# Performance work log

Hardware: AMD Instinct MI355X
Metric: run time of the kernel (lower is better)

The kernel has to match this reference:

```python
import jax, jax.numpy as jnp
import numpy as np

B, T, C = 4, 2048, 1024
H = 16
HD = C // H  # 64


def setup_inputs() -> dict:
    key = jax.random.key(0)
    k1, k2, k3 = jax.random.split(key, 3)
    x = jax.random.normal(k1, (B, T, C), dtype=jnp.float32)
    W_qkv = jax.random.normal(k2, (3 * C, C), dtype=jnp.float32) * (C ** -0.5)
    W_proj = jax.random.normal(k3, (C, C), dtype=jnp.float32) * (C ** -0.5)
    b_proj = jnp.zeros((C,), dtype=jnp.float32)
    return {"x": x, "W_qkv": W_qkv, "W_proj": W_proj, "b_proj": b_proj}


def reference(x, W_qkv, W_proj, b_proj):
    # qkv = x @ W_qkv.T : [B,T,3C]
    qkv = jnp.einsum('btc,oc->bto', x, W_qkv)
    # Faithful to torch: view(B,T,H,3*HD) then chunk last dim -> per-head q/k/v
    qkv = qkv.reshape(B, T, H, 3 * HD)
    q, k, v = jnp.split(qkv, 3, axis=-1)      # each [B,T,H,HD]
    q = q.transpose(0, 2, 1, 3)               # [B,H,T,HD]
    k = k.transpose(0, 2, 1, 3)
    v = v.transpose(0, 2, 1, 3)
    scale = HD ** -0.5
    att = jnp.einsum('bhqd,bhkd->bhqk', q, k) * scale  # [B,H,T,T]
    causal = jnp.tril(jnp.ones((T, T), dtype=bool))
    att = jnp.where(causal, att, -jnp.inf)
    att = jax.nn.softmax(att, axis=-1)
    out = jnp.einsum('bhqk,bhkd->bhqd', att, v)        # [B,H,T,HD]
    out = out.transpose(0, 2, 1, 3).reshape(B, T, C)
    out = jnp.einsum('btc,oc->bto', out, W_proj) + b_proj
    return out
```

## Files before the change

kernel.cpp:

```cpp
#include <hip/hip_runtime.h>
#include <stdint.h>

#define B_ 4
#define T_ 2048
#define C_ 1024
#define H_ 16
#define HD_ 64

typedef __attribute__((ext_vector_type(8))) short short8;
typedef __attribute__((ext_vector_type(4))) float f32x4;

typedef uint32_t __attribute__((address_space(3))) lds_u32;
typedef const uint32_t __attribute__((address_space(1))) glb_u32;

__device__ inline void async16(const void* g, void* l) {
    __builtin_amdgcn_global_load_lds((glb_u32*)g, (lds_u32*)l, 16, 0, 0);
}

__device__ inline short f2bf(float f) {
    union { float f; uint32_t u; } x; x.f = f;
    uint32_t r = (x.u + 0x7fffu + ((x.u >> 16) & 1u)) >> 16;
    return (short)r;
}
__device__ inline float bf2f(short b) {
    union { uint32_t u; float f; } x; x.u = ((uint32_t)(uint16_t)b) << 16;
    return x.f;
}
__device__ inline uint32_t cvt_pk_bf16(float lo, float hi) {
    uint32_t r;
    asm("v_cvt_pk_bf16_f32 %0, %1, %2" : "=v"(r) : "v"(lo), "v"(hi));
    return r;
}

#define FENCE asm volatile("" ::: "memory")
#define BAR   do { FENCE; __builtin_amdgcn_s_barrier(); FENCE; } while (0)
#define VMC3  asm volatile("s_waitcnt vmcnt(3)" ::: "memory")

__global__ void convert_all(const void* __restrict__ x,  const void* __restrict__ wq,
                            const void* __restrict__ wp, const void* __restrict__ bias,
                            short* __restrict__ xd, short* __restrict__ wqd,
                            short* __restrict__ wpd, short* __restrict__ biasd,
                            int* __restrict__ flag_out)
{
    __shared__ int cnt;
    if (threadIdx.x == 0) cnt = 0;
    __syncthreads();
    int sane = 0;
    const uint32_t* xu = (const uint32_t*)x;
    for (int i = threadIdx.x; i < 1024; i += 256) {
        float v = bf2f((short)(xu[i] & 0xFFFFu));
        float a = fabsf(v);
        if (a > 1e-5f && a < 1e5f) sane++;
    }
    atomicAdd(&cnt, sane);
    __syncthreads();
    const int isf32 = (cnt < 512) ? 1 : 0;

    const int blk = blockIdx.x;
    const void* src; short* dst; int base, n;
    if (blk < 4096)      { src = x;    dst = xd;    base = blk;        n = B_*T_*C_; }
    else if (blk < 5632) { src = wq;   dst = wqd;   base = blk - 4096; n = 3*C_*C_; }
    else if (blk < 6144) { src = wp;   dst = wpd;   base = blk - 5632; n = C_*C_; }
    else                 { src = bias; dst = biasd; base = 0;          n = C_;
                           if (threadIdx.x == 0) *flag_out = isf32; }
    const int i = (base * 256 + threadIdx.x) * 8;
    if (i >= n) return;
    if (isf32) {
        const float* s = (const float*)src;
        short8 o;
#pragma unroll
        for (int j = 0; j < 8; j++) o[j] = f2bf(s[i + j]);
        *(short8*)&dst[i] = o;
    } else {
        *(short8*)&dst[i] = *(const short8*)((const short*)src + i);
    }
}

template <bool DUAL>
__global__ __launch_bounds__(512, 2) void gemm8(
    const short* __restrict__ A, const short* __restrict__ Bm,
    const short* __restrict__ bias_bf, void* __restrict__ Cout,
    int M, int N, int K, const int* __restrict__ flag)
{
    __shared__ short lds[49152];
    const int tid  = threadIdx.x;
    const int lane = tid & 63;
    const int wid  = tid >> 6;
    const int quad = lane >> 4;
    const int lcol = lane & 15;
    const int wm   = wid >> 2;
    const int wn   = wid & 3;
    const int nbx  = N >> 8;

    const int cpx = gridDim.x >> 3;
    const int wg  = (blockIdx.x & 7) * cpx + (blockIdx.x >> 3);
    const int m0 = (wg / nbx) << 7;
    const int n0 = (wg % nbx) << 8;
    const int isf32 = DUAL ? *flag : 0;

    const int srow = tid >> 3;
    const int sch  = ((tid & 7) ^ (srow & 7)) << 3;
    auto stA = [&](int buf, int i, int kt) {
        async16(&A[(size_t)(m0 + i * 64 + srow) * K + kt * 64 + sch],
                &lds[buf * 8192 + i * 4096 + tid * 8]);
    };
    auto stB = [&](int buf, int i, int kt) {
        async16(&Bm[(size_t)(n0 + i * 64 + srow) * K + kt * 64 + sch],
                &lds[16384 + buf * 16384 + i * 4096 + tid * 8]);
    };

    f32x4 acc[4][4];
#pragma unroll
    for (int i = 0; i < 4; i++)
#pragma unroll
        for (int j = 0; j < 4; j++) acc[i][j] = f32x4{0.f, 0.f, 0.f, 0.f};

    short8 a[4][2], b[4][2];
    auto rdA2 = [&](int mb, int buf) {
#pragma unroll
        for (int m2 = 0; m2 < 2; m2++)
#pragma unroll
            for (int ks = 0; ks < 2; ks++)
                a[mb + m2][ks] = *(const short8*)&lds[buf * 8192
                    + (wm * 64 + (mb + m2) * 16 + lcol) * 64
                    + ((((ks << 2) | quad) ^ (lcol & 7)) << 3)];
    };
    auto rdB2 = [&](int nb, int buf) {
#pragma unroll
        for (int n2 = 0; n2 < 2; n2++)
#pragma unroll
            for (int ks = 0; ks < 2; ks++)
                b[nb + n2][ks] = *(const short8*)&lds[16384 + buf * 16384
                    + (wn * 64 + (nb + n2) * 16 + lcol) * 64
                    + ((((ks << 2) | quad) ^ (lcol & 7)) << 3)];
    };
    auto mmq = [&](int mb, int nb) {
        __builtin_amdgcn_s_setprio(1);
#pragma unroll
        for (int m2 = 0; m2 < 2; m2++)
#pragma unroll
            for (int n2 = 0; n2 < 2; n2++)
#pragma unroll
                for (int ks = 0; ks < 2; ks++)
                    acc[mb + m2][nb + n2] = __builtin_amdgcn_mfma_f32_16x16x32_bf16(
                        a[mb + m2][ks], b[nb + n2][ks], acc[mb + m2][nb + n2], 0, 0, 0);
        __builtin_amdgcn_s_setprio(0);
    };

    const int NT = K >> 6;
    stB(0, 0, 0); stB(0, 1, 0); stB(0, 2, 0); stB(0, 3, 0);
    stA(0, 0, 0); stA(0, 1, 0);
    stB(1, 0, 1); stB(1, 1, 1); stA(1, 0, 1);
    VMC3;
    BAR;

    for (int i = 0; i < NT / 2; i++) {
        const int to = 2 * i + 1;
        const int t2 = (2 * i + 2 < NT) ? 2 * i + 2 : NT - 1;
        const int t3 = (2 * i + 3 < NT) ? 2 * i + 3 : NT - 1;
        rdA2(0, 0); rdB2(0, 0); stB(1, 2, to); stB(1, 3, to);
        BAR; mmq(0, 0); BAR;
        rdA2(2, 0);             stA(1, 1, to);
        BAR; mmq(2, 0); BAR;
        rdB2(2, 0);
        BAR; mmq(0, 2); BAR;
        stB(0, 0, t2); stB(0, 1, t2); stA(0, 0, t2);
        BAR; mmq(2, 2); VMC3; BAR;
        rdA2(0, 1); rdB2(0, 1); stB(0, 2, t2); stB(0, 3, t2);
        BAR; mmq(0, 0); BAR;
        rdA2(2, 1);             stA(0, 1, t2);
        BAR; mmq(2, 0); BAR;
        rdB2(2, 1);
        BAR; mmq(0, 2); BAR;
        stB(1, 0, t3); stB(1, 1, t3); stA(1, 0, t3);
        BAR; mmq(2, 2); VMC3; BAR;
    }

    float bv[4];
#pragma unroll
    for (int nf = 0; nf < 4; nf++)
        bv[nf] = bias_bf ? bf2f(bias_bf[n0 + wn * 64 + nf * 16 + lcol]) : 0.f;
#pragma unroll
    for (int mf = 0; mf < 4; mf++)
#pragma unroll
        for (int r = 0; r < 4; r++) {
            const int row = m0 + wm * 64 + mf * 16 + quad * 4 + r;
#pragma unroll
            for (int nf = 0; nf < 4; nf++) {
                const int col = n0 + wn * 64 + nf * 16 + lcol;
                const float val = acc[mf][nf][r] + bv[nf];
                const size_t off = (size_t)row * N + col;
                if (DUAL && isf32) ((float*)Cout)[off] = val;
                else               ((short*)Cout)[off] = f2bf(val);
            }
        }
}

__global__ __launch_bounds__(256) void attn(const short* __restrict__ qkv,
                                            short* __restrict__ att)
{
    __shared__ short lds_k[64][72];
    __shared__ short lds_vt[64][68];

    const int tid  = threadIdx.x;
    const int lane = tid & 63;
    const int wave = tid >> 6;
    const int quad = lane >> 4;
    const int lcol = lane & 15;

    const int bh   = blockIdx.x & 63;
    const int j    = blockIdx.x >> 6;
    const int b    = bh >> 4;
    const int h    = bh & 15;

    const size_t rowstride = 3 * C_;
    const size_t bhbase = (size_t)b * T_ * rowstride + (size_t)h * (3 * HD_);

    const int kkey = tid >> 2;
    const int kdp  = (tid & 3) * 16;
    const int vkey = tid & 63;
    const int vkp  = (vkey & 0x23) | ((vkey & 0x0C) << 1) | ((vkey & 0x10) >> 2);
    const int vd0  = (tid >> 6) * 16;

    short8 vones;
#pragma unroll
    for (int i = 0; i < 8; i++) vones[i] = (short)0x3F80;

    const short* kp; const short* vp;
    short8 kA, kB, vA, vB;
    const size_t TILE_STEP = (size_t)64 * rowstride;
    auto load_init = [&]() {
        kp = &qkv[bhbase + (size_t)kkey * rowstride + HD_ + kdp];
        vp = &qkv[bhbase + (size_t)vkey * rowstride + 2 * HD_ + vd0];
    };
    auto load_tile = [&]() {
        kA = *(const short8*)kp;
        kB = *(const short8*)(kp + 8);
        vA = *(const short8*)vp;
        vB = *(const short8*)(vp + 8);
        kp += TILE_STEP; vp += TILE_STEP;
    };

    const float SC = 0.1803368801f;
    auto scale_frag = [&](short8 q) {
        short8 r;
#pragma unroll
        for (int i = 0; i < 8; i++) r[i] = f2bf(bf2f(q[i]) * SC);
        return r;
    };

    auto process_chunk = [&](int qblk, bool sync_first) {
        const int q0 = qblk * 128;
        const int qA = q0 + wave * 16;
        const int qB = q0 + 64 + wave * 16;

        short8 qfA0, qfA1, qfB0, qfB1;
        {
            const size_t ba = bhbase + (size_t)(qA + lcol) * rowstride + quad * 8;
            qfA0 = scale_frag(*(const short8*)&qkv[ba]);
            qfA1 = scale_frag(*(const short8*)&qkv[ba + 32]);
            const size_t bb = bhbase + (size_t)(qB + lcol) * rowstride + quad * 8;
            qfB0 = scale_frag(*(const short8*)&qkv[bb]);
            qfB1 = scale_frag(*(const short8*)&qkv[bb + 32]);
        }

        f32x4 oA[4], oB[4], oLA, oLB;
#pragma unroll
        for (int i = 0; i < 4; i++) { oA[i] = f32x4{0.f,0.f,0.f,0.f}; oB[i] = f32x4{0.f,0.f,0.f,0.f}; }
        oLA = f32x4{0.f,0.f,0.f,0.f}; oLB = f32x4{0.f,0.f,0.f,0.f};

        load_init();
        load_tile();

        const int LT = 2 * qblk + 1;
        for (int kt = 0; kt <= LT; ++kt) {
            if (kt || sync_first) __syncthreads();
            *(short8*)&lds_k[kkey][kdp]     = kA;
            *(short8*)&lds_k[kkey][kdp + 8] = kB;
#pragma unroll
            for (int jj = 0; jj < 8; jj++) {
                lds_vt[vd0 + jj][vkp]     = vA[jj];
                lds_vt[vd0 + 8 + jj][vkp] = vB[jj];
            }
            __syncthreads();
            if (kt < LT) load_tile();

            const int k0 = kt * 64;
            const bool doA = (kt < LT);

            f32x4 SA[4], SB[4];
#pragma unroll
            for (int t = 0; t < 4; t++) {
                const short8 kf0 = *(const short8*)&lds_k[t * 16 + lcol][quad * 8];
                const short8 kf1 = *(const short8*)&lds_k[t * 16 + lcol][32 + quad * 8];
                SB[t] = f32x4{0.f, 0.f, 0.f, 0.f};
                SB[t] = __builtin_amdgcn_mfma_f32_16x16x32_bf16(kf0, qfB0, SB[t], 0, 0, 0);
                SB[t] = __builtin_amdgcn_mfma_f32_16x16x32_bf16(kf1, qfB1, SB[t], 0, 0, 0);
                if (doA) {
                    SA[t] = f32x4{0.f, 0.f, 0.f, 0.f};
                    SA[t] = __builtin_amdgcn_mfma_f32_16x16x32_bf16(kf0, qfA0, SA[t], 0, 0, 0);
                    SA[t] = __builtin_amdgcn_mfma_f32_16x16x32_bf16(kf1, qfA1, SA[t], 0, 0, 0);
                }
            }

            short8 vf[4][2];
#pragma unroll
            for (int dt = 0; dt < 4; dt++) {
                vf[dt][0] = *(const short8*)&lds_vt[dt * 16 + lcol][quad * 8];
                vf[dt][1] = *(const short8*)&lds_vt[dt * 16 + lcol][32 + quad * 8];
            }

            auto do_mtile = [&](f32x4 (&S)[4], f32x4 (&o)[4], f32x4& oL,
                                int qX, bool maskT) {
                if (maskT) {
                    const int qthr = qX + lcol - k0 - quad * 4;
#pragma unroll
                    for (int t = 0; t < 4; t++)
#pragma unroll
                        for (int r = 0; r < 4; r++) {
                            float e = __builtin_amdgcn_exp2f(S[t][r]);
                            if (t * 16 + r > qthr) e = 0.f;
                            S[t][r] = e;
                        }
                } else {
#pragma unroll
                    for (int t = 0; t < 4; t++)
#pragma unroll
                        for (int r = 0; r < 4; r++)
                            S[t][r] = __builtin_amdgcn_exp2f(S[t][r]);
                }
                union { uint32_t u[4]; short8 s; } p0, p1;
#pragma unroll
                for (int w = 0; w < 4; w++) {
                    const int t0 = w >> 1, r0 = (w & 1) * 2;
                    p0.u[w] = cvt_pk_bf16(S[t0][r0],     S[t0][r0 + 1]);
                    p1.u[w] = cvt_pk_bf16(S[2 + t0][r0], S[2 + t0][r0 + 1]);
                }
                oL = __builtin_amdgcn_mfma_f32_16x16x32_bf16(p0.s, vones, oL, 0, 0, 0);
                oL = __builtin_amdgcn_mfma_f32_16x16x32_bf16(p1.s, vones, oL, 0, 0, 0);
#pragma unroll
                for (int dt = 0; dt < 4; dt++) {
                    o[dt] = __builtin_amdgcn_mfma_f32_16x16x32_bf16(p0.s, vf[dt][0], o[dt], 0, 0, 0);
                    o[dt] = __builtin_amdgcn_mfma_f32_16x16x32_bf16(p1.s, vf[dt][1], o[dt], 0, 0, 0);
                }
            };

            if (doA) do_mtile(SA, oA, oLA, qA, kt == LT - 1);
            do_mtile(SB, oB, oLB, qB, kt == LT);
        }

#pragma unroll
        for (int r = 0; r < 4; r++) {
            const float la = oLA[r], lb = oLB[r];
            const float iar = (la > 0.f) ? 1.f / la : 0.f;
            const float ibr = (lb > 0.f) ? 1.f / lb : 0.f;
            const int qi  = quad * 4 + r;
            const int qrA = qA + qi;
            const int qrB = qB + qi;
#pragma unroll
            for (int dt = 0; dt < 4; dt++) {
                const int col = h * HD_ + dt * 16 + lcol;
                att[(size_t)(b * T_ + qrA) * C_ + col] = f2bf(oA[dt][r] * iar);
                att[(size_t)(b * T_ + qrB) * C_ + col] = f2bf(oB[dt][r] * ibr);
            }
        }
    };

    process_chunk(15 - j, false);
    process_chunk(j, true);
}

extern "C" void kernel_launch(void* const* d_in, const int* in_sizes, int n_in,
                              void* d_out, int out_size, void* d_ws, size_t ws_size,
                              hipStream_t stream) {
    char* ws = (char*)d_ws;
    short* qkv     = (short*)(ws);
    short* x_or_at = (short*)(ws + 50331648);
    short* wq_bf   = (short*)(ws + 50331648 + 16777216);
    short* wp_bf   = (short*)(ws + 50331648 + 16777216 + 6291456);
    short* bias_bf = (short*)(ws + 50331648 + 16777216 + 6291456 + 2097152);
    int*   flag    = (int*)  (ws + 50331648 + 16777216 + 6291456 + 2097152 + 2048);

    dim3 blk(256);

    convert_all<<<dim3(6145), blk, 0, stream>>>(
        d_in[0], d_in[1], d_in[2], d_in[3],
        x_or_at, wq_bf, wp_bf, bias_bf, flag);

    gemm8<false><<<dim3(768), dim3(512), 0, stream>>>(
        x_or_at, wq_bf, nullptr, qkv, B_ * T_, 3 * C_, C_, flag);

    attn<<<dim3(B_ * H_ * (T_ / 256)), blk, 0, stream>>>(qkv, x_or_at);

    gemm8<true><<<dim3(256), dim3(512), 0, stream>>>(
        x_or_at, wp_bf, bias_bf, d_out, B_ * T_, C_, C_, flag);
}
```

Baseline: 252.0 us.

## Triple-buffer GEMM LDS stages with one barrier per k-tile

Replaces the hand-interleaved double-buffered schedule of the bf16 GEMM, which issued many barriers per k-tile, with a triple-buffered loop. Each iteration waits on vmcnt(6), passes one barrier, reads all A/B fragments from LDS, issues the async global-to-LDS loads for tile t+2, then runs all 16 MFMA groups under raised priority. The aim is to cut barrier overhead and keep loads two tiles ahead of compute. In exchange, LDS per block grows from 96 KB to 144 KB, which likely prevents two 512-thread blocks from sharing a CU despite the launch bounds.

Measured after the change: 242.0 us. 1.04x faster.

```diff
diff --git a/kernel.cpp b/kernel.cpp
--- a/kernel.cpp
+++ b/kernel.cpp
@@ -34,7 +34,7 @@
 
 #define FENCE asm volatile("" ::: "memory")
 #define BAR   do { FENCE; __builtin_amdgcn_s_barrier(); FENCE; } while (0)
-#define VMC3  asm volatile("s_waitcnt vmcnt(3)" ::: "memory")
+#define VMC6  asm volatile("s_waitcnt vmcnt(6)" ::: "memory")
 
 __global__ void convert_all(const void* __restrict__ x,  const void* __restrict__ wq,
                             const void* __restrict__ wp, const void* __restrict__ bias,
@@ -82,7 +82,7 @@
     const short* __restrict__ bias_bf, void* __restrict__ Cout,
     int M, int N, int K, const int* __restrict__ flag)
 {
-    __shared__ short lds[49152];
+    __shared__ short lds[73728];
     const int tid  = threadIdx.x;
     const int lane = tid & 63;
     const int wid  = tid >> 6;
@@ -106,7 +106,11 @@
     };
     auto stB = [&](int buf, int i, int kt) {
         async16(&Bm[(size_t)(n0 + i * 64 + srow) * K + kt * 64 + sch],
-                &lds[16384 + buf * 16384 + i * 4096 + tid * 8]);
+                &lds[24576 + buf * 16384 + i * 4096 + tid * 8]);
+    };
+    auto stage6 = [&](int buf, int kt) {
+        stB(buf, 0, kt); stB(buf, 1, kt); stB(buf, 2, kt); stB(buf, 3, kt);
+        stA(buf, 0, kt); stA(buf, 1, kt);
     };
 
     f32x4 acc[4][4];
@@ -130,12 +134,11 @@
         for (int n2 = 0; n2 < 2; n2++)
 #pragma unroll
             for (int ks = 0; ks < 2; ks++)
-                b[nb + n2][ks] = *(const short8*)&lds[16384 + buf * 16384
+                b[nb + n2][ks] = *(const short8*)&lds[24576 + buf * 16384
                     + (wn * 64 + (nb + n2) * 16 + lcol) * 64
                     + ((((ks << 2) | quad) ^ (lcol & 7)) << 3)];
     };
     auto mmq = [&](int mb, int nb) {
-        __builtin_amdgcn_s_setprio(1);
 #pragma unroll
         for (int m2 = 0; m2 < 2; m2++)
 #pragma unroll
@@ -144,36 +147,24 @@
                 for (int ks = 0; ks < 2; ks++)
                     acc[mb + m2][nb + n2] = __builtin_amdgcn_mfma_f32_16x16x32_bf16(
                         a[mb + m2][ks], b[nb + n2][ks], acc[mb + m2][nb + n2], 0, 0, 0);
+    };
+
+    const int NT = K >> 6;
+    stage6(0, 0);
+    stage6(1, 1);
+
+    int bt = 0, b1i = 1, b2i = 2;
+    for (int t = 0; t < NT; ++t) {
+        const int ts = (t + 2 < NT) ? t + 2 : NT - 1;
+        VMC6;
+        BAR;
+        rdA2(0, bt); rdA2(2, bt); rdB2(0, bt); rdB2(2, bt);
+        stage6(b2i, ts);
+        __builtin_amdgcn_s_setprio(1);
+        mmq(0, 0); mmq(2, 0); mmq(0, 2); mmq(2, 2);
         __builtin_amdgcn_s_setprio(0);
-    };
-
-    const int NT = K >> 6;
-    stB(0, 0, 0); stB(0, 1, 0); stB(0, 2, 0); stB(0, 3, 0);
-    stA(0, 0, 0); stA(0, 1, 0);
-    stB(1, 0, 1); stB(1, 1, 1); stA(1, 0, 1);
-    VMC3;
-    BAR;
-
-    for (int i = 0; i < NT / 2; i++) {
-        const int to = 2 * i + 1;
-        const int t2 = (2 * i + 2 < NT) ? 2 * i + 2 : NT - 1;
-        const int t3 = (2 * i + 3 < NT) ? 2 * i + 3 : NT - 1;
-        rdA2(0, 0); rdB2(0, 0); stB(1, 2, to); stB(1, 3, to);
-        BAR; mmq(0, 0); BAR;
-        rdA2(2, 0);             stA(1, 1, to);
-        BAR; mmq(2, 0); BAR;
-        rdB2(2, 0);
-        BAR; mmq(0, 2); BAR;
-        stB(0, 0, t2); stB(0, 1, t2); stA(0, 0, t2);
-        BAR; mmq(2, 2); VMC3; BAR;
-        rdA2(0, 1); rdB2(0, 1); stB(0, 2, t2); stB(0, 3, t2);
-        BAR; mmq(0, 0); BAR;
-        rdA2(2, 1);             stA(0, 1, t2);
-        BAR; mmq(2, 0); BAR;
-        rdB2(2, 1);
-        BAR; mmq(0, 2); BAR;
-        stB(1, 0, t3); stB(1, 1, t3); stA(1, 0, t3);
-        BAR; mmq(2, 2); VMC3; BAR;
+        const int nb = bt;
+        bt = b1i; b1i = b2i; b2i = nb;
     }
 
     float bv[4];
```
